# Performance work log

Hardware: AMD Instinct MI355X
Metric: run time of the kernel (lower is better)

Reference implementation:

```python
import jax, jax.numpy as jnp
import numpy as np
import itertools

WIDTH, HEIGHT = 32, 32


def _build_freudenthal(width, height):
    """Static structure of the Freudenthal triangulation of a width x height grid.
    Returns (verts[n,3], faces[n,3], dims[n]) as numpy int32; verts padded by
    repeating the first vertex (harmless under max), faces padded with -1.
    Vertices are appended first so simplex index of vertex v equals v."""
    simplices = []
    for i in range(height):
        for j in range(width):
            simplices.append((i * width + j,))
    for i in range(height):
        for j in range(width - 1):
            ind = i * width + j
            simplices.append((ind, ind + 1))
    for i in range(height - 1):
        for j in range(width):
            ind = i * width + j
            simplices.append((ind, ind + width))
    for i in range(height - 1):
        for j in range(width - 1):
            ind = i * width + j
            simplices.append((ind, ind + width + 1))
            simplices.append((ind, ind + 1, ind + width + 1))
            simplices.append((ind, ind + width, ind + width + 1))
    index = {frozenset(s): k for k, s in enumerate(simplices)}
    n = len(simplices)
    verts = np.zeros((n, 3), np.int32)
    faces = np.full((n, 3), -1, np.int32)
    dims = np.zeros(n, np.int32)
    for k, s in enumerate(simplices):
        d = len(s) - 1
        dims[k] = d
        vs = list(s) + [s[0]] * (3 - len(s))
        verts[k] = vs
        if d > 0:
            for m, fc in enumerate(itertools.combinations(s, len(s) - 1)):
                faces[k, m] = index[frozenset(fc)]
    return verts, faces, dims


def setup_inputs() -> dict:
    key = jax.random.key(0)
    f = jax.random.normal(key, (HEIGHT, WIDTH), dtype=jnp.float32)
    verts, faces, dims = _build_freudenthal(WIDTH, HEIGHT)
    cap1 = int((dims == 1).sum())  # upper bound on number of H1 bars
    return {
        "f": f,
        "verts": jnp.asarray(verts),
        "faces": jnp.asarray(faces),
        "dims": jnp.asarray(dims),
        "cap1": cap1,
    }


def _persistence(f, verts, faces, dims, cap1):
    n = verts.shape[0]
    V = f.size
    iota = jnp.arange(n, dtype=jnp.int32)
    fv = f.reshape(-1)
    # lower-star filtration: simplex value = max over its vertices (grad -> argmax vertex)
    fs = jnp.max(fv[verts], axis=1)
    # sort simplices by filtration value, ties broken by dimension (faces first)
    order = jnp.lexsort((dims, fs))
    rank = jnp.zeros(n, jnp.int32).at[order].set(iota)
    fs_s = fs[order]
    dims_s = dims[order]
    # Z2 boundary matrix in sorted order: R[rank[face], rank[simplex]] = 1
    col_idx = jnp.broadcast_to(rank[:, None], (n, 3))
    row_idx = jnp.where(faces >= 0, rank[jnp.clip(faces, 0)], n)
    R0 = jnp.zeros((n, n), jnp.int8).at[row_idx, col_idx].set(1, mode='drop')
    pivot0 = jnp.full(n, -1, jnp.int32)  # pivot[i] = column whose low is row i

    def low_of(col):
        return jnp.max(jnp.where(col != 0, iota, -1))

    def reduce_col(j, state):
        R, pivot = state

        def cond(col):
            l = low_of(col)
            return jnp.where(l >= 0, pivot[l], -1) >= 0

        def body(col):
            return jnp.bitwise_xor(col, R[:, pivot[low_of(col)]])

        col = jax.lax.while_loop(cond, body, R[:, j])
        R = R.at[:, j].set(col)
        l = low_of(col)
        pivot = pivot.at[jnp.where(l >= 0, l, n)].set(j, mode='drop')
        return R, pivot

    R, pivot = jax.lax.fori_loop(0, n, reduce_col, (R0, pivot0))
    lows = jnp.max(jnp.where(R != 0, iota[:, None], -1), axis=0)
    is_birth = lows == -1          # zero (reduced) columns create homology classes
    paired = pivot >= 0
    births = fs_s
    deaths = jnp.where(paired, fs_s[jnp.clip(pivot, 0)], jnp.inf)

    def pack(mask, cap):
        pos = jnp.cumsum(mask) - 1
        rows = jnp.where(mask, pos, cap)
        out = jnp.zeros((cap, 2), f.dtype)
        out = out.at[rows, 0].set(jnp.where(mask, births, 0.0), mode='drop')
        out = out.at[rows, 1].set(jnp.where(mask, deaths, 0.0), mode='drop')
        return out

    dgm0 = pack(is_birth & (dims_s == 0), V)     # exactly V dim-0 bars
    dgm1 = pack(is_birth & (dims_s == 1), cap1)  # padded with (0,0)
    return dgm0, dgm1


_persistence_jit = jax.jit(_persistence, static_argnums=(4,))


def reference(f, verts, faces, dims, cap1):
    # sublevel=True path of LevelSetLayer2D.forward: (dgms, True); we return the dgms
    return _persistence_jit(f, verts, faces, dims, cap1)
```

## Files before the change

### kernel.cpp

```cpp
#include <hip/hip_runtime.h>


#define Wd 32
#define Hd 32
#define NV 1024
#define NHE 992
#define NVE 992
#define NE 2945
#define NT 1922
#define OUTERN 1922
#define DBASE 3008
#define CAP1 2945

typedef unsigned long long ull;

__device__ __forceinline__ float clampf(float x) {
  return fminf(fmaxf(x, -1e37f), 1e37f);
}

__device__ __forceinline__ int ldw(int* p) {
  return __hip_atomic_load(p, __ATOMIC_RELAXED, __HIP_MEMORY_SCOPE_WORKGROUP);
}
__device__ __forceinline__ void stw(int* p, int v) {
  __hip_atomic_store(p, v, __ATOMIC_RELAXED, __HIP_MEMORY_SCOPE_WORKGROUP);
}

__device__ __forceinline__ void edge_decode(int e, int &u, int &v, int &fa, int &fb) {
  if (e < NHE) {
    int i = e / (Wd - 1), j = e - i * (Wd - 1);
    u = i * Wd + j; v = u + 1;
    fa = (i < Hd - 1) ? 2 * (i * (Wd - 1) + j) : OUTERN;
    fb = (i > 0) ? 2 * ((i - 1) * (Wd - 1) + j) + 1 : OUTERN;
  } else if (e < NHE + NVE) {
    int k = e - NHE;
    int i = k / Wd, j = k - i * Wd;
    u = i * Wd + j; v = u + Wd;
    fa = (j < Wd - 1) ? 2 * (i * (Wd - 1) + j) + 1 : OUTERN;
    fb = (j > 0) ? 2 * (i * (Wd - 1) + j - 1) : OUTERN;
  } else {
    int c = e - NHE - NVE;
    int i = c / (Wd - 1), j = c - i * (Wd - 1);
    u = i * Wd + j; v = u + Wd + 1;
    fa = 2 * c; fb = 2 * c + 1;
  }
}

__device__ __forceinline__ int block_excl_scan512(int val, int tid, int* tmp) {
  int lane = tid & 63, wv = tid >> 6;
  int s = val;
  for (int off = 1; off < 64; off <<= 1) {
    int t = __shfl_up(s, off);
    if (lane >= off) s += t;
  }
  if (lane == 63) tmp[wv] = s;
  __syncthreads();
  if (wv == 0) {
    int w = (lane < 8) ? tmp[lane] : 0;
    for (int off = 1; off < 8; off <<= 1) {
      int t = __shfl_up(w, off);
      if (lane >= off) w += t;
    }
    if (lane < 8) tmp[lane] = w;
  }
  __syncthreads();
  int wbase = (wv > 0) ? tmp[wv - 1] : 0;
  return wbase + s - val;
}

__global__ __launch_bounds__(512, 1)
void ph_fused(const float* __restrict__ f, float* __restrict__ out) {
  __shared__ __align__(16) float fv[NV];
  __shared__ int rvx[NV];
  __shared__ __align__(16) unsigned char scratch[NV * 6 * 2];
  __shared__ float deaths0[NV];
  __shared__ int par0[NV];
  __shared__ unsigned clAV[NV];
  __shared__ int par2[NT + 1];
  __shared__ unsigned bkey2[NT + 1];
  __shared__ float bfs2[NT + 1];
  __shared__ unsigned clAT[NT + 1];
  __shared__ unsigned seUV[NE];
  __shared__ float sefs[NE];
  __shared__ unsigned seF[NE];
  __shared__ float deth[NE];
  __shared__ int posflag[NE];
  __shared__ int cntE[NV];
  __shared__ int scanbuf[16];
  __shared__ int cons, nact;

  ull* skey = (ull*)scratch;
  unsigned short* bufEid = (unsigned short*)scratch;

  const int tid = (int)threadIdx.x;
  const int isDual = (int)blockIdx.x;

  {
    float a = f[tid], b = f[tid + 512];
    fv[tid] = a; fv[tid + 512] = b;
    unsigned ua = __float_as_uint(a == 0.0f ? 0.0f : a);
    ua = (ua & 0x80000000u) ? ~ua : (ua | 0x80000000u);
    unsigned ub = __float_as_uint(b == 0.0f ? 0.0f : b);
    ub = (ub & 0x80000000u) ? ~ub : (ub | 0x80000000u);
    skey[tid] = ((ull)ua << 32) | (unsigned)tid;
    skey[tid + 512] = ((ull)ub << 32) | (unsigned)(tid + 512);
    if (tid == 0) { cons = 512; nact = NE; }
  }
  __syncthreads();

  for (int k = 2; k <= NV; k <<= 1) {
    for (int j = k >> 1; j >= 1; j >>= 1) {
      if (k >= 128 && j >= 32 && j <= 256) __syncthreads();
      else __builtin_amdgcn_wave_barrier();
      #pragma unroll
      for (int h = 0; h < 2; ++h) {
        int t = tid + h * 512;
        int p = t ^ j;
        if (p > t) {
          bool up = ((t & k) == 0);
          ull a = skey[t], b = skey[p];
          if ((a > b) == up) { skey[t] = b; skey[p] = a; }
        }
      }
    }
  }
  __syncthreads();
  #pragma unroll
  for (int h = 0; h < 2; ++h) {
    int r = tid + h * 512;
    int v = (int)(skey[r] & 0xffffffffu);
    rvx[v] = r;
    cntE[r] = 0;
    if (!isDual) {
      out[2 * r] = clampf(fv[v]);
      deaths0[r] = 1e37f;
      par0[r] = r;
      clAV[r] = 0u;
    }
  }
  __syncthreads();

  for (int e = tid; e < NE; e += 512) {
    int u, v, fa, fb;
    edge_decode(e, u, v, fa, fb);
    int b = max(rvx[u], rvx[v]);
    int slot = atomicAdd(&cntE[b], 1);
    bufEid[b * 6 + slot] = (unsigned short)e;
    if (isDual) posflag[e] = 0;
  }
  if (isDual) {
    for (int t = tid; t < NT; t += 512) {
      int c = t >> 1, s = t & 1;
      int ci = c / (Wd - 1), cj = c - ci * (Wd - 1);
      int a0 = ci * Wd + cj;
      int v1 = s ? (a0 + Wd) : (a0 + 1);
      int v2 = a0 + Wd + 1;
      int r = max(rvx[a0], max(rvx[v1], rvx[v2]));
      float fm = fmaxf(fv[a0], fmaxf(fv[v1], fv[v2]));
      par2[t] = t;
      bkey2[t] = ((unsigned)r << 14) | (1u << 13) | (unsigned)(DBASE + 3 * c + 1 + s);
      bfs2[t] = fm;
      clAT[t] = 0u;
    }
    if (tid == 0) {
      par2[OUTERN] = OUTERN;
      bkey2[OUTERN] = 0xFFFFFFFFu;
      bfs2[OUTERN] = 0.0f;
      clAT[OUTERN] = 0u;
    }
    for (int q = tid; q < 2 * CAP1; q += 512) out[2 * NV + q] = 0.0f;
  }
  __syncthreads();

  {
    int b0 = 2 * tid, b1 = 2 * tid + 1;
    int c0 = cntE[b0], c1 = cntE[b1];
    int base0 = block_excl_scan512(c0 + c1, tid, scanbuf);
    #pragma unroll
    for (int h = 0; h < 2; ++h) {
      int b = h ? b1 : b0;
      int cnt = h ? c1 : c0;
      int base = h ? (base0 + c0) : base0;
      for (int k = 1; k < cnt; ++k) {
        unsigned short key = bufEid[b * 6 + k];
        int m = k - 1;
        while (m >= 0 && bufEid[b * 6 + m] > key) {
          bufEid[b * 6 + m + 1] = bufEid[b * 6 + m];
          --m;
        }
        bufEid[b * 6 + m + 1] = key;
      }
      for (int k = 0; k < cnt; ++k) {
        int e = (int)bufEid[b * 6 + k];
        int u, v, fa, fb;
        edge_decode(e, u, v, fa, fb);
        int pos = base + k;
        sefs[pos] = fmaxf(fv[u], fv[v]);
        if (!isDual) seUV[pos] = (unsigned)rvx[u] | ((unsigned)rvx[v] << 16);
        else         seF[pos]  = (unsigned)fa | ((unsigned)fb << 16);
      }
    }
  }
  __syncthreads();

  if (!isDual) {
    int have = 1, pend = 0;
    int e = tid, x, y, D = 0, S = 0;
    unsigned myenc = 0;
    { unsigned uv = seUV[e]; x = (int)(uv & 0xffffu); y = (int)(uv >> 16); }
    unsigned roundc = 1;
    for (;;) {
      if (have) {
        for (;;) {
          for (;;) {
            int px = ldw(&par0[x]), py = ldw(&par0[y]);
            if (px == x && py == y) break;
            int gx = ldw(&par0[px]), gy = ldw(&par0[py]);
            if (px != x) stw(&par0[x], gx);
            if (py != y) stw(&par0[y], gy);
            x = gx; y = gy;
          }
          if (x != y) {
            myenc = (roundc << 12) | (4095u - (unsigned)e);
            D = max(x, y); S = min(x, y);
            atomicMax(&clAV[D], myenc);
            atomicMax(&clAV[S], myenc);
            pend = 1;
            break;
          }
          atomicSub(&nact, 1);
          int ne = atomicAdd(&cons, 1);
          if (ne < NE) {
            e = ne;
            unsigned uv = seUV[e]; x = (int)(uv & 0xffffu); y = (int)(uv >> 16);
          } else { have = 0; break; }
        }
      }
      __syncthreads();
      if (have && pend) {
        if (clAV[D] == myenc) {
          stw(&par0[D], S);
          deaths0[D] = sefs[e];
          atomicSub(&nact, 1);
          int ne = atomicAdd(&cons, 1);
          if (ne < NE) {
            e = ne;
            unsigned uv = seUV[e]; x = (int)(uv & 0xffffu); y = (int)(uv >> 16);
          } else have = 0;
        }
        pend = 0;
      }
      __syncthreads();
      if (ldw(&nact) == 0) break;
      roundc++;
    }
  } else {
    int have = 1, pend = 0;
    int e = NE - 1 - tid, x, y, D = 0, S = 0;
    unsigned myenc = 0;
    { unsigned ff = seF[e]; x = (int)(ff & 0xffffu); y = (int)(ff >> 16); }
    unsigned roundc = 1;
    for (;;) {
      if (have) {
        for (;;) {
          for (;;) {
            int px = ldw(&par2[x]), py = ldw(&par2[y]);
            if (px == x && py == y) break;
            int gx = ldw(&par2[px]), gy = ldw(&par2[py]);
            if (px != x) stw(&par2[x], gx);
            if (py != y) stw(&par2[y], gy);
            x = gx; y = gy;
          }
          if (x != y) {
            myenc = (roundc << 12) | (unsigned)(e + 1);
            unsigned kx = bkey2[x], ky = bkey2[y];
            D = (kx < ky) ? x : y;
            S = (kx < ky) ? y : x;
            atomicMax(&clAT[D], myenc);
            atomicMax(&clAT[S], myenc);
            pend = 1;
            break;
          }
          atomicSub(&nact, 1);
          int ne = atomicAdd(&cons, 1);
          if (ne < NE) {
            e = NE - 1 - ne;
            unsigned ff = seF[e]; x = (int)(ff & 0xffffu); y = (int)(ff >> 16);
          } else { have = 0; break; }
        }
      }
      __syncthreads();
      if (have && pend) {
        if (clAT[D] == myenc) {
          stw(&par2[D], S);
          posflag[e] = 1;
          deth[e] = bfs2[D];
          atomicSub(&nact, 1);
          int ne = atomicAdd(&cons, 1);
          if (ne < NE) {
            e = NE - 1 - ne;
            unsigned ff = seF[e]; x = (int)(ff & 0xffffu); y = (int)(ff >> 16);
          } else have = 0;
        }
        pend = 0;
      }
      __syncthreads();
      if (ldw(&nact) == 0) break;
      roundc++;
    }
  }
  __syncthreads();

  if (!isDual) {
    out[2 * tid + 1] = clampf(deaths0[tid]);
    out[2 * (tid + 512) + 1] = clampf(deaths0[tid + 512]);
  } else {
    int q0 = 6 * tid;
    int cc[6];
    int csum = 0;
    #pragma unroll
    for (int m = 0; m < 6; ++m) {
      int q = q0 + m;
      cc[m] = (q < NE) ? posflag[q] : 0;
      csum += cc[m];
    }
    int p = block_excl_scan512(csum, tid, scanbuf);
    #pragma unroll
    for (int m = 0; m < 6; ++m) {
      if (cc[m]) {
        out[2 * NV + 2 * p] = clampf(sefs[q0 + m]);
        out[2 * NV + 2 * p + 1] = clampf(deth[q0 + m]);
        p++;
      }
    }
  }
}

extern "C" void kernel_launch(void* const* d_in, const int* in_sizes, int n_in,
                              void* d_out, int out_size, void* d_ws, size_t ws_size,
                              hipStream_t stream) {
  const float* f = (const float*)d_in[0];
  float* out = (float*)d_out;
  hipLaunchKernelGGL(ph_fused, dim3(2), dim3(512), 0, stream, f, out);
}
```

Baseline: 102.9 us.

## Hand off tail of union-find merge rounds to a single wavefront

Once the number of active edges drops to a threshold, the remaining work items are queued in shared memory. One 64-thread wavefront then finishes the parallel Kruskal-style union-find rounds using wave barriers instead of block-wide __syncthreads. It also caps how many already-merged edges a thread consumes per round, so rounds stay balanced. This targets the cost of many block barriers during the long serial tail, at the risk of subtle correctness issues from intra-wave ordering of shared-memory atomics.

```diff
diff --git a/kernel.cpp b/kernel.cpp
--- a/kernel.cpp
+++ b/kernel.cpp
@@ -11,6 +11,8 @@
 #define OUTERN 1922
 #define DBASE 3008
 #define CAP1 2945
+#define SOLO_T 56
+#define EAT_CAP 8
 
 typedef unsigned long long ull;
 
@@ -86,7 +88,8 @@
   __shared__ int posflag[NE];
   __shared__ int cntE[NV];
   __shared__ int scanbuf[16];
-  __shared__ int cons, nact;
+  __shared__ int qbuf[64];
+  __shared__ int cons, nact, qn;
 
   ull* skey = (ull*)scratch;
   unsigned short* bufEid = (unsigned short*)scratch;
@@ -103,7 +106,7 @@
     ub = (ub & 0x80000000u) ? ~ub : (ub | 0x80000000u);
     skey[tid] = ((ull)ua << 32) | (unsigned)tid;
     skey[tid + 512] = ((ull)ub << 32) | (unsigned)(tid + 512);
-    if (tid == 0) { cons = 512; nact = NE; }
+    if (tid == 0) { cons = 512; nact = NE; qn = 0; }
   }
   __syncthreads();
 
@@ -210,6 +213,7 @@
     unsigned roundc = 1;
     for (;;) {
       if (have) {
+        int eat = 0;
         for (;;) {
           for (;;) {
             int px = ldw(&par0[x]), py = ldw(&par0[y]);
@@ -229,10 +233,10 @@
           }
           atomicSub(&nact, 1);
           int ne = atomicAdd(&cons, 1);
-          if (ne < NE) {
-            e = ne;
-            unsigned uv = seUV[e]; x = (int)(uv & 0xffffu); y = (int)(uv >> 16);
-          } else { have = 0; break; }
+          if (ne >= NE) { have = 0; break; }
+          e = ne;
+          unsigned uv = seUV[e]; x = (int)(uv & 0xffffu); y = (int)(uv >> 16);
+          if (++eat >= EAT_CAP) break;
         }
       }
       __syncthreads();
@@ -250,8 +254,73 @@
         pend = 0;
       }
       __syncthreads();
-      if (ldw(&nact) == 0) break;
+      int na = ldw(&nact);
+      if (na == 0) break;
       roundc++;
+      if (na <= SOLO_T) {
+        if (have) { int s = atomicAdd(&qn, 1); qbuf[s] = e; }
+        __syncthreads();
+        if (tid >= 64) break;
+        int qc = ldw(&qn);
+        pend = 0;
+        if (tid < qc) {
+          e = qbuf[tid]; have = 1;
+          unsigned uv = seUV[e]; x = (int)(uv & 0xffffu); y = (int)(uv >> 16);
+        } else {
+          int ne = atomicAdd(&cons, 1);
+          if (ne < NE) {
+            e = ne; have = 1;
+            unsigned uv = seUV[e]; x = (int)(uv & 0xffffu); y = (int)(uv >> 16);
+          } else have = 0;
+        }
+        for (;;) {
+          if (have) {
+            int eat = 0;
+            for (;;) {
+              for (;;) {
+                int px = ldw(&par0[x]), py = ldw(&par0[y]);
+                if (px == x && py == y) break;
+                int gx = ldw(&par0[px]), gy = ldw(&par0[py]);
+                if (px != x) stw(&par0[x], gx);
+                if (py != y) stw(&par0[y], gy);
+                x = gx; y = gy;
+              }
+              if (x != y) {
+                myenc = (roundc << 12) | (4095u - (unsigned)e);
+                D = max(x, y); S = min(x, y);
+                atomicMax(&clAV[D], myenc);
+                atomicMax(&clAV[S], myenc);
+                pend = 1;
+                break;
+              }
+              atomicSub(&nact, 1);
+              int ne = atomicAdd(&cons, 1);
+              if (ne >= NE) { have = 0; break; }
+              e = ne;
+              unsigned uv = seUV[e]; x = (int)(uv & 0xffffu); y = (int)(uv >> 16);
+              if (++eat >= EAT_CAP) break;
+            }
+          }
+          __builtin_amdgcn_wave_barrier();
+          if (have && pend) {
+            if (clAV[D] == myenc) {
+              stw(&par0[D], S);
+              deaths0[D] = sefs[e];
+              atomicSub(&nact, 1);
+              int ne = atomicAdd(&cons, 1);
+              if (ne < NE) {
+                e = ne;
+                unsigned uv = seUV[e]; x = (int)(uv & 0xffffu); y = (int)(uv >> 16);
+              } else have = 0;
+            }
+            pend = 0;
+          }
+          __builtin_amdgcn_wave_barrier();
+          if (ldw(&nact) == 0) break;
+          roundc++;
+        }
+        break;
+      }
     }
   } else {
     int have = 1, pend = 0;
@@ -261,6 +330,7 @@
     unsigned roundc = 1;
     for (;;) {
       if (have) {
+        int eat = 0;
         for (;;) {
           for (;;) {
             int px = ldw(&par2[x]), py = ldw(&par2[y]);
@@ -282,10 +352,10 @@
           }
           atomicSub(&nact, 1);
           int ne = atomicAdd(&cons, 1);
-          if (ne < NE) {
-            e = NE - 1 - ne;
-            unsigned ff = seF[e]; x = (int)(ff & 0xffffu); y = (int)(ff >> 16);
-          } else { have = 0; break; }
+          if (ne >= NE) { have = 0; break; }
+          e = NE - 1 - ne;
+          unsigned ff = seF[e]; x = (int)(ff & 0xffffu); y = (int)(ff >> 16);
+          if (++eat >= EAT_CAP) break;
         }
       }
       __syncthreads();
@@ -304,8 +374,76 @@
         pend = 0;
       }
       __syncthreads();
-      if (ldw(&nact) == 0) break;
+      int na = ldw(&nact);
+      if (na == 0) break;
       roundc++;
+      if (na <= SOLO_T) {
+        if (have) { int s = atomicAdd(&qn, 1); qbuf[s] = e; }
+        __syncthreads();
+        if (tid >= 64) break;
+        int qc = ldw(&qn);
+        pend = 0;
+        if (tid < qc) {
+          e = qbuf[tid]; have = 1;
+          unsigned ff = seF[e]; x = (int)(ff & 0xffffu); y = (int)(ff >> 16);
+        } else {
+          int ne = atomicAdd(&cons, 1);
+          if (ne < NE) {
+            e = NE - 1 - ne; have = 1;
+            unsigned ff = seF[e]; x = (int)(ff & 0xffffu); y = (int)(ff >> 16);
+          } else have = 0;
+        }
+        for (;;) {
+          if (have) {
+            int eat = 0;
+            for (;;) {
+              for (;;) {
+                int px = ldw(&par2[x]), py = ldw(&par2[y]);
+                if (px == x && py == y) break;
+                int gx = ldw(&par2[px]), gy = ldw(&par2[py]);
+                if (px != x) stw(&par2[x], gx);
+                if (py != y) stw(&par2[y], gy);
+                x = gx; y = gy;
+              }
+              if (x != y) {
+                myenc = (roundc << 12) | (unsigned)(e + 1);
+                unsigned kx = bkey2[x], ky = bkey2[y];
+                D = (kx < ky) ? x : y;
+                S = (kx < ky) ? y : x;
+                atomicMax(&clAT[D], myenc);
+                atomicMax(&clAT[S], myenc);
+                pend = 1;
+                break;
+              }
+              atomicSub(&nact, 1);
+              int ne = atomicAdd(&cons, 1);
+              if (ne >= NE) { have = 0; break; }
+              e = NE - 1 - ne;
+              unsigned ff = seF[e]; x = (int)(ff & 0xffffu); y = (int)(ff >> 16);
+              if (++eat >= EAT_CAP) break;
+            }
+          }
+          __builtin_amdgcn_wave_barrier();
+          if (have && pend) {
+            if (clAT[D] == myenc) {
+              stw(&par2[D], S);
+              posflag[e] = 1;
+              deth[e] = bfs2[D];
+              atomicSub(&nact, 1);
+              int ne = atomicAdd(&cons, 1);
+              if (ne < NE) {
+                e = NE - 1 - ne;
+                unsigned ff = seF[e]; x = (int)(ff & 0xffffu); y = (int)(ff >> 16);
+              } else have = 0;
+            }
+            pend = 0;
+          }
+          __builtin_amdgcn_wave_barrier();
+          if (ldw(&nact) == 0) break;
+          roundc++;
+        }
+        break;
+      }
     }
   }
   __syncthreads();
```

Result: no change. 104.0 us (+1.0%).

## Process two edges per thread in the union-find conflict rounds

Applied to the files above, without the earlier changes.

Each thread now carries two in-flight edges (A and B) through the round-based parallel union-find for both the primal (H0) and dual (H1) passes. The initial consumer counter starts at 1024 so 1024 edges are active per round instead of 512. The intent is to resolve more merges per barrier-separated round, cutting the number of rounds and __syncthreads, and to overlap the latency of the two find chains. In exchange it raises register use and branch divergence, and more simultaneous claims may cause more atomicMax conflicts and retries.

```diff
diff --git a/kernel.cpp b/kernel.cpp
--- a/kernel.cpp
+++ b/kernel.cpp
@@ -103,7 +103,7 @@
     ub = (ub & 0x80000000u) ? ~ub : (ub | 0x80000000u);
     skey[tid] = ((ull)ua << 32) | (unsigned)tid;
     skey[tid + 512] = ((ull)ub << 32) | (unsigned)(tid + 512);
-    if (tid == 0) { cons = 512; nact = NE; }
+    if (tid == 0) { cons = 2 * 512; nact = NE; }
   }
   __syncthreads();
 
@@ -203,105 +203,162 @@
   __syncthreads();
 
   if (!isDual) {
-    int have = 1, pend = 0;
-    int e = tid, x, y, D = 0, S = 0;
-    unsigned myenc = 0;
-    { unsigned uv = seUV[e]; x = (int)(uv & 0xffffu); y = (int)(uv >> 16); }
+    int hvA = 1, pdA = 0, eA = tid, xA, yA, DA = 0, SA = 0;
+    int hvB = 1, pdB = 0, eB = 512 + tid, xB, yB, DB = 0, SB = 0;
+    unsigned encA = 0, encB = 0;
+    { unsigned uv = seUV[eA]; xA = (int)(uv & 0xffffu); yA = (int)(uv >> 16); }
+    { unsigned uv = seUV[eB]; xB = (int)(uv & 0xffffu); yB = (int)(uv >> 16); }
     unsigned roundc = 1;
     for (;;) {
-      if (have) {
-        for (;;) {
-          for (;;) {
-            int px = ldw(&par0[x]), py = ldw(&par0[y]);
-            if (px == x && py == y) break;
-            int gx = ldw(&par0[px]), gy = ldw(&par0[py]);
-            if (px != x) stw(&par0[x], gx);
-            if (py != y) stw(&par0[y], gy);
-            x = gx; y = gy;
+      pdA = 0; pdB = 0;
+      int fA = hvA, fB = hvB;
+      while (fA | fB) {
+        int pxA, pyA, pxB, pyB;
+        if (fA) { pxA = ldw(&par0[xA]); pyA = ldw(&par0[yA]); }
+        if (fB) { pxB = ldw(&par0[xB]); pyB = ldw(&par0[yB]); }
+        if (fA) {
+          if (pxA == xA && pyA == yA) {
+            if (xA != yA) {
+              encA = (roundc << 12) | (4095u - (unsigned)eA);
+              DA = max(xA, yA); SA = min(xA, yA);
+              atomicMax(&clAV[DA], encA);
+              atomicMax(&clAV[SA], encA);
+              pdA = 1; fA = 0;
+            } else {
+              atomicSub(&nact, 1);
+              int ne = atomicAdd(&cons, 1);
+              if (ne >= NE) { hvA = 0; fA = 0; }
+              else { eA = ne; unsigned uv = seUV[eA]; xA = (int)(uv & 0xffffu); yA = (int)(uv >> 16); }
+            }
+          } else {
+            int gx = ldw(&par0[pxA]), gy = ldw(&par0[pyA]);
+            if (pxA != xA) stw(&par0[xA], gx);
+            if (pyA != yA) stw(&par0[yA], gy);
+            xA = gx; yA = gy;
           }
-          if (x != y) {
-            myenc = (roundc << 12) | (4095u - (unsigned)e);
-            D = max(x, y); S = min(x, y);
-            atomicMax(&clAV[D], myenc);
-            atomicMax(&clAV[S], myenc);
-            pend = 1;
-            break;
+        }
+        if (fB) {
+          if (pxB == xB && pyB == yB) {
+            if (xB != yB) {
+              encB = (roundc << 12) | (4095u - (unsigned)eB);
+              DB = max(xB, yB); SB = min(xB, yB);
+              atomicMax(&clAV[DB], encB);
+              atomicMax(&clAV[SB], encB);
+              pdB = 1; fB = 0;
+            } else {
+              atomicSub(&nact, 1);
+              int ne = atomicAdd(&cons, 1);
+              if (ne >= NE) { hvB = 0; fB = 0; }
+              else { eB = ne; unsigned uv = seUV[eB]; xB = (int)(uv & 0xffffu); yB = (int)(uv >> 16); }
+            }
+          } else {
+            int gx = ldw(&par0[pxB]), gy = ldw(&par0[pyB]);
+            if (pxB != xB) stw(&par0[xB], gx);
+            if (pyB != yB) stw(&par0[yB], gy);
+            xB = gx; yB = gy;
           }
-          atomicSub(&nact, 1);
-          int ne = atomicAdd(&cons, 1);
-          if (ne < NE) {
-            e = ne;
-            unsigned uv = seUV[e]; x = (int)(uv & 0xffffu); y = (int)(uv >> 16);
-          } else { have = 0; break; }
         }
       }
       __syncthreads();
-      if (have && pend) {
-        if (clAV[D] == myenc) {
-          stw(&par0[D], S);
-          deaths0[D] = sefs[e];
-          atomicSub(&nact, 1);
-          int ne = atomicAdd(&cons, 1);
-          if (ne < NE) {
-            e = ne;
-            unsigned uv = seUV[e]; x = (int)(uv & 0xffffu); y = (int)(uv >> 16);
-          } else have = 0;
-        }
-        pend = 0;
+      if (pdA && clAV[DA] == encA) {
+        stw(&par0[DA], SA);
+        deaths0[DA] = sefs[eA];
+        atomicSub(&nact, 1);
+        int ne = atomicAdd(&cons, 1);
+        if (ne < NE) { eA = ne; unsigned uv = seUV[eA]; xA = (int)(uv & 0xffffu); yA = (int)(uv >> 16); }
+        else hvA = 0;
+      }
+      if (pdB && clAV[DB] == encB) {
+        stw(&par0[DB], SB);
+        deaths0[DB] = sefs[eB];
+        atomicSub(&nact, 1);
+        int ne = atomicAdd(&cons, 1);
+        if (ne < NE) { eB = ne; unsigned uv = seUV[eB]; xB = (int)(uv & 0xffffu); yB = (int)(uv >> 16); }
+        else hvB = 0;
       }
       __syncthreads();
       if (ldw(&nact) == 0) break;
       roundc++;
     }
   } else {
-    int have = 1, pend = 0;
-    int e = NE - 1 - tid, x, y, D = 0, S = 0;
-    unsigned myenc = 0;
-    { unsigned ff = seF[e]; x = (int)(ff & 0xffffu); y = (int)(ff >> 16); }
+    int hvA = 1, pdA = 0, eA = NE - 1 - tid, xA, yA, DA = 0, SA = 0;
+    int hvB = 1, pdB = 0, eB = NE - 1 - (512 + tid), xB, yB, DB = 0, SB = 0;
+    unsigned encA = 0, encB = 0;
+    { unsigned ff = seF[eA]; xA = (int)(ff & 0xffffu); yA = (int)(ff >> 16); }
+    { unsigned ff = seF[eB]; xB = (int)(ff & 0xffffu); yB = (int)(ff >> 16); }
     unsigned roundc = 1;
     for (;;) {
-      if (have) {
-        for (;;) {
-          for (;;) {
-            int px = ldw(&par2[x]), py = ldw(&par2[y]);
-            if (px == x && py == y) break;
-            int gx = ldw(&par2[px]), gy = ldw(&par2[py]);
-            if (px != x) stw(&par2[x], gx);
-            if (py != y) stw(&par2[y], gy);
-            x = gx; y = gy;
+      pdA = 0; pdB = 0;
+      int fA = hvA, fB = hvB;
+      while (fA | fB) {
+        int pxA, pyA, pxB, pyB;
+        if (fA) { pxA = ldw(&par2[xA]); pyA = ldw(&par2[yA]); }
+        if (fB) { pxB = ldw(&par2[xB]); pyB = ldw(&par2[yB]); }
+        if (fA) {
+          if (pxA == xA && pyA == yA) {
+            if (xA != yA) {
+              encA = (roundc << 12) | (unsigned)(eA + 1);
+              unsigned kx = bkey2[xA], ky = bkey2[yA];
+              DA = (kx < ky) ? xA : yA;
+              SA = (kx < ky) ? yA : xA;
+              atomicMax(&clAT[DA], encA);
+              atomicMax(&clAT[SA], encA);
+              pdA = 1; fA = 0;
+            } else {
+              atomicSub(&nact, 1);
+              int ne = atomicAdd(&cons, 1);
+              if (ne >= NE) { hvA = 0; fA = 0; }
+              else { eA = NE - 1 - ne; unsigned ff = seF[eA]; xA = (int)(ff & 0xffffu); yA = (int)(ff >> 16); }
+            }
+          } else {
+            int gx = ldw(&par2[pxA]), gy = ldw(&par2[pyA]);
+            if (pxA != xA) stw(&par2[xA], gx);
+            if (pyA != yA) stw(&par2[yA], gy);
+            xA = gx; yA = gy;
           }
-          if (x != y) {
-            myenc = (roundc << 12) | (unsigned)(e + 1);
-            unsigned kx = bkey2[x], ky = bkey2[y];
-            D = (kx < ky) ? x : y;
-            S = (kx < ky) ? y : x;
-            atomicMax(&clAT[D], myenc);
-            atomicMax(&clAT[S], myenc);
-            pend = 1;
-            break;
+        }
+        if (fB) {
+          if (pxB == xB && pyB == yB) {
+            if (xB != yB) {
+              encB = (roundc << 12) | (unsigned)(eB + 1);
+              unsigned kx = bkey2[xB], ky = bkey2[yB];
+              DB = (kx < ky) ? xB : yB;
+              SB = (kx < ky) ? yB : xB;
+              atomicMax(&clAT[DB], encB);
+              atomicMax(&clAT[SB], encB);
+              pdB = 1; fB = 0;
+            } else {
+              atomicSub(&nact, 1);
+              int ne = atomicAdd(&cons, 1);
+              if (ne >= NE) { hvB = 0; fB = 0; }
+              else { eB = NE - 1 - ne; unsigned ff = seF[eB]; xB = (int)(ff & 0xffffu); yB = (int)(ff >> 16); }
+            }
+          } else {
+            int gx = ldw(&par2[pxB]), gy = ldw(&par2[pyB]);
+            if (pxB != xB) stw(&par2[xB], gx);
+            if (pyB != yB) stw(&par2[yB], gy);
+            xB = gx; yB = gy;
           }
-          atomicSub(&nact, 1);
-          int ne = atomicAdd(&cons, 1);
-          if (ne < NE) {
-            e = NE - 1 - ne;
-            unsigned ff = seF[e]; x = (int)(ff & 0xffffu); y = (int)(ff >> 16);
-          } else { have = 0; break; }
         }
       }
       __syncthreads();
-      if (have && pend) {
-        if (clAT[D] == myenc) {
-          stw(&par2[D], S);
-          posflag[e] = 1;
-          deth[e] = bfs2[D];
-          atomicSub(&nact, 1);
-          int ne = atomicAdd(&cons, 1);
-          if (ne < NE) {
-            e = NE - 1 - ne;
-            unsigned ff = seF[e]; x = (int)(ff & 0xffffu); y = (int)(ff >> 16);
-          } else have = 0;
-        }
-        pend = 0;
+      if (pdA && clAT[DA] == encA) {
+        stw(&par2[DA], SA);
+        posflag[eA] = 1;
+        deth[eA] = bfs2[DA];
+        atomicSub(&nact, 1);
+        int ne = atomicAdd(&cons, 1);
+        if (ne < NE) { eA = NE - 1 - ne; unsigned ff = seF[eA]; xA = (int)(ff & 0xffffu); yA = (int)(ff >> 16); }
+        else hvA = 0;
+      }
+      if (pdB && clAT[DB] == encB) {
+        stw(&par2[DB], SB);
+        posflag[eB] = 1;
+        deth[eB] = bfs2[DB];
+        atomicSub(&nact, 1);
+        int ne = atomicAdd(&cons, 1);
+        if (ne < NE) { eB = NE - 1 - ne; unsigned ff = seF[eB]; xB = (int)(ff & 0xffffu); yB = (int)(ff >> 16); }
+        else hvB = 0;
       }
       __syncthreads();
       if (ldw(&nact) == 0) break;
```

Measured after the change: 109.2 us. +6.1%, slower.
